# Kernel optimization log

Measured on AMD Instinct MI355X. Metric: run time of the kernel, lower is better.

Reference implementation:

```python
import jax, jax.numpy as jnp
import numpy as np

BETA = 0.99
EPS = 1e-05


def setup_inputs() -> dict:
    key = jax.random.key(0)
    s = jax.random.normal(key, (16, 2000, 257, 2), dtype=jnp.float32)
    return {"s": s}


def reference(s):
    # s: (N, T, F, C). Unbiased EWMA mean/var normalization, sequential over T.
    N, T, F, C = s.shape
    st = jnp.transpose(s, (1, 0, 2, 3))  # (T, N, F, C) for scan over time
    zeros = jnp.zeros((N, F, C), dtype=s.dtype)
    one = jnp.asarray(1.0, dtype=s.dtype)
    beta = jnp.asarray(BETA, dtype=s.dtype)

    def step(carry, x):
        beta_t, v1, v2, S = carry
        beta_t = beta * beta_t
        v1 = beta * v1 + (1 - beta) * x
        v2_prev = v2
        v2 = v1 / (1 - beta_t)
        w = (1 - beta) / (1 - beta_t)
        S = (1 - w) * S + w * (x - v2) * (x - v2_prev)
        S = S * (S > 0)  # clamp negative variance to 0 (as in original)
        y = (x - v2) / jnp.sqrt(S + EPS)
        return (beta_t, v1, v2, S), y

    init = (one, zeros, zeros, zeros)
    _, out = jax.lax.scan(step, init, st)
    return jnp.transpose(out, (1, 0, 2, 3))  # back to (N, T, F, C)
```

## Files before the change

### kernel.cpp

```cpp
#include <hip/hip_runtime.h>


#define NN 16
#define TT 2000
#define FCC 514
#define SERIES (NN * FCC)
#define EPSF 1e-5f
#define NCHUNK 7
#define CLEN 286
#define WARM 512
#define PF 16
#define MAXL 800

__global__ __launch_bounds__(64)
void ewma_kernel(const float* __restrict__ s, float* __restrict__ out) {
    __shared__ float4 tab[MAXL];

    const int chunk = blockIdx.y;
    const int t_out = chunk * CLEN;
    int t_end = t_out + CLEN; if (t_end > TT) t_end = TT;
    int t0 = t_out - WARM;     if (t0 < 0) t0 = 0;
    const int L = t_end - t0;

    {
        double bd = 0.99, acc = 1.0;
        int e = t0 + 1 + (int)threadIdx.x;
        while (e) { if (e & 1) acc *= bd; bd *= bd; e >>= 1; }
        double b64 = 0.99;
        for (int i = 0; i < 6; ++i) b64 *= b64;
        for (int j = (int)threadIdx.x; j < L; j += 64) {
            const float om = (float)(1.0 - acc);
            const float r  = __builtin_amdgcn_rcpf(om);
            const float w  = 0.01f * r;
            tab[j] = make_float4(r, w, 1.0f - w, 0.0f);
            acc *= b64;
        }
    }
    __syncthreads();

    const int tid = blockIdx.x * 64 + (int)threadIdx.x;
    if (tid >= SERIES) return;

    const int n  = tid / FCC;
    const int fc = tid - n * FCC;
    const size_t base = (size_t)n * TT * FCC + (size_t)fc + (size_t)t0 * FCC;
    const float* p  = s   + base;
    float*       po = out + base;

    float v1 = 0.0f, v2p = 0.0f, S = 0.0f;

    float buf[PF];
    #pragma unroll
    for (int i = 0; i < PF; ++i) buf[i] = p[i * FCC];

    int t = t0, j = 0;
    while (t + PF <= t_end) {
        const float* pf_ptr = (t + 2 * PF <= t_end) ? (p + PF * FCC) : p;
        float nbuf[PF];
        #pragma unroll
        for (int i = 0; i < PF; ++i) nbuf[i] = pf_ptr[i * FCC];

        const bool full_out = (t >= t_out);
        #pragma unroll
        for (int i = 0; i < PF; ++i) {
            const float4 tw = tab[j + i];
            const float x  = buf[i];
            v1 = fmaf(0.99f, v1, 0.01f * x);
            const float v2 = v1 * tw.x;
            const float d  = x - v2;
            const float pr = d * (x - v2p);
            S = fmaxf(fmaf(tw.z, S, tw.y * pr), 0.0f);
            const float y = d * __builtin_amdgcn_rsqf(S + EPSF);
            v2p = v2;
            if (full_out || (t + i >= t_out)) po[i * FCC] = y;
        }

        #pragma unroll
        for (int i = 0; i < PF; ++i) buf[i] = nbuf[i];
        p  += PF * FCC;
        po += PF * FCC;
        t  += PF;
        j  += PF;
    }
    for (; t < t_end; ++t, ++j) {
        const float4 tw = tab[j];
        const float x  = *p;
        v1 = fmaf(0.99f, v1, 0.01f * x);
        const float v2 = v1 * tw.x;
        const float d  = x - v2;
        const float pr = d * (x - v2p);
        S = fmaxf(fmaf(tw.z, S, tw.y * pr), 0.0f);
        const float y = d * __builtin_amdgcn_rsqf(S + EPSF);
        v2p = v2;
        if (t >= t_out) *po = y;
        p  += FCC;
        po += FCC;
    }
}

extern "C" void kernel_launch(void* const* d_in, const int* in_sizes, int n_in,
                              void* d_out, int out_size, void* d_ws, size_t ws_size,
                              hipStream_t stream) {
    const float* s = (const float*)d_in[0];
    float* out = (float*)d_out;
    dim3 grid((SERIES + 63) / 64, NCHUNK);
    ewma_kernel<<<grid, dim3(64), 0, stream>>>(s, out);
}
```

Measured before the change: 162.1 us.

## Stage time tiles through double-buffered LDS with cooperative float2 loads per batch

Each block now handles one batch element and one time chunk (16x16 grid, 576 threads). Threads cooperatively load contiguous tiles of 14 time steps x 514 features into double-buffered shared memory with float2 loads, while 514 threads run the recurrence out of LDS. Time chunks shrink to 125 steps with the same 512-step warmup, so redundant warmup work grows considerably in exchange for more parallelism and coalesced bulk loads. The weight table is reduced to float2 and the S update is rewritten as S + w*(pr - S).

```diff
diff --git a/kernel.cpp b/kernel.cpp
--- a/kernel.cpp
+++ b/kernel.cpp
@@ -1,100 +1,113 @@
 #include <hip/hip_runtime.h>
 
 
-#define NN 16
-#define TT 2000
-#define FCC 514
-#define SERIES (NN * FCC)
+#define NN   16
+#define TT   2000
+#define FCC  514
 #define EPSF 1e-5f
-#define NCHUNK 7
-#define CLEN 286
+#define KCH  16
+#define CLEN 125
 #define WARM 512
-#define PF 16
-#define MAXL 800
+#define TILE 14
+#define BLK  576
+#define MAXL (CLEN + WARM)
+#define ITER 7
 
-__global__ __launch_bounds__(64)
+__global__ __launch_bounds__(BLK)
 void ewma_kernel(const float* __restrict__ s, float* __restrict__ out) {
-    __shared__ float4 tab[MAXL];
+    __shared__ float  buf[2][TILE * FCC];
+    __shared__ float2 tab[MAXL];
 
-    const int chunk = blockIdx.y;
-    const int t_out = chunk * CLEN;
-    int t_end = t_out + CLEN; if (t_end > TT) t_end = TT;
-    int t0 = t_out - WARM;     if (t0 < 0) t0 = 0;
-    const int L = t_end - t0;
+    const int tid = (int)threadIdx.x;
+    const int c   = (int)blockIdx.x;
+    const int n   = (int)blockIdx.y;
+
+    const int t_out = c * CLEN;
+    const int t_end = t_out + CLEN;
+    int t0 = t_out - WARM; if (t0 < 0) t0 = 0;
+    const int L    = t_end - t0;
+    const int jout = t_out - t0;
+
+    for (int j = tid; j < L; j += BLK) {
+        double bd = 0.99, acc = 1.0;
+        int e = t0 + 1 + j;
+        while (e) { if (e & 1) acc *= bd; bd *= bd; e >>= 1; }
+        const float om = (float)(1.0 - acc);
+        const float r  = __builtin_amdgcn_rcpf(om);
+        tab[j] = make_float2(r, 0.01f * r);
+    }
+
+    const size_t base = (size_t)n * TT * FCC + (size_t)t0 * FCC;
+    const float* sb = s   + base;
+    float*       ob = out + base;
+
+    const int ntile = (L + TILE - 1) / TILE;
+
+    float2 pre[ITER];
 
     {
-        double bd = 0.99, acc = 1.0;
-        int e = t0 + 1 + (int)threadIdx.x;
-        while (e) { if (e & 1) acc *= bd; bd *= bd; e >>= 1; }
-        double b64 = 0.99;
-        for (int i = 0; i < 6; ++i) b64 *= b64;
-        for (int j = (int)threadIdx.x; j < L; j += 64) {
-            const float om = (float)(1.0 - acc);
-            const float r  = __builtin_amdgcn_rcpf(om);
-            const float w  = 0.01f * r;
-            tab[j] = make_float4(r, w, 1.0f - w, 0.0f);
-            acc *= b64;
+        const int navail = (L < TILE ? L : TILE) * FCC;
+        #pragma unroll
+        for (int it = 0; it < ITER; ++it) {
+            const int o = tid * 2 + it * (BLK * 2);
+            if (o < navail) pre[it] = *(const float2*)(sb + o);
+        }
+        #pragma unroll
+        for (int it = 0; it < ITER; ++it) {
+            const int o = tid * 2 + it * (BLK * 2);
+            if (o < navail) *(float2*)&buf[0][o] = pre[it];
         }
     }
     __syncthreads();
 
-    const int tid = blockIdx.x * 64 + (int)threadIdx.x;
-    if (tid >= SERIES) return;
+    float v1 = 0.f, v2p = 0.f, S = 0.f;
 
-    const int n  = tid / FCC;
-    const int fc = tid - n * FCC;
-    const size_t base = (size_t)n * TT * FCC + (size_t)fc + (size_t)t0 * FCC;
-    const float* p  = s   + base;
-    float*       po = out + base;
+    for (int k = 0; k < ntile; ++k) {
+        const int b    = k & 1;
+        const int rows = (L - k * TILE < TILE) ? (L - k * TILE) : TILE;
 
-    float v1 = 0.0f, v2p = 0.0f, S = 0.0f;
-
-    float buf[PF];
-    #pragma unroll
-    for (int i = 0; i < PF; ++i) buf[i] = p[i * FCC];
-
-    int t = t0, j = 0;
-    while (t + PF <= t_end) {
-        const float* pf_ptr = (t + 2 * PF <= t_end) ? (p + PF * FCC) : p;
-        float nbuf[PF];
-        #pragma unroll
-        for (int i = 0; i < PF; ++i) nbuf[i] = pf_ptr[i * FCC];
-
-        const bool full_out = (t >= t_out);
-        #pragma unroll
-        for (int i = 0; i < PF; ++i) {
-            const float4 tw = tab[j + i];
-            const float x  = buf[i];
-            v1 = fmaf(0.99f, v1, 0.01f * x);
-            const float v2 = v1 * tw.x;
-            const float d  = x - v2;
-            const float pr = d * (x - v2p);
-            S = fmaxf(fmaf(tw.z, S, tw.y * pr), 0.0f);
-            const float y = d * __builtin_amdgcn_rsqf(S + EPSF);
-            v2p = v2;
-            if (full_out || (t + i >= t_out)) po[i * FCC] = y;
+        int nnext = 0;
+        if (k + 1 < ntile) {
+            const int rn = (L - (k + 1) * TILE < TILE) ? (L - (k + 1) * TILE) : TILE;
+            nnext = rn * FCC;
+            const float* g = sb + (size_t)(k + 1) * TILE * FCC;
+            #pragma unroll
+            for (int it = 0; it < ITER; ++it) {
+                const int o = tid * 2 + it * (BLK * 2);
+                if (o < nnext) pre[it] = *(const float2*)(g + o);
+            }
         }
 
-        #pragma unroll
-        for (int i = 0; i < PF; ++i) buf[i] = nbuf[i];
-        p  += PF * FCC;
-        po += PF * FCC;
-        t  += PF;
-        j  += PF;
-    }
-    for (; t < t_end; ++t, ++j) {
-        const float4 tw = tab[j];
-        const float x  = *p;
-        v1 = fmaf(0.99f, v1, 0.01f * x);
-        const float v2 = v1 * tw.x;
-        const float d  = x - v2;
-        const float pr = d * (x - v2p);
-        S = fmaxf(fmaf(tw.z, S, tw.y * pr), 0.0f);
-        const float y = d * __builtin_amdgcn_rsqf(S + EPSF);
-        v2p = v2;
-        if (t >= t_out) *po = y;
-        p  += FCC;
-        po += FCC;
+        if (tid < FCC) {
+            const float* tp = &buf[b][tid];
+            float*       op = ob + (size_t)k * TILE * FCC + tid;
+            const int jb = k * TILE;
+            #pragma unroll
+            for (int r = 0; r < TILE; ++r) {
+                if (r < rows) {
+                    const float2 tw = tab[jb + r];
+                    const float x  = tp[r * FCC];
+                    v1 = fmaf(0.99f, v1, 0.01f * x);
+                    const float v2 = v1 * tw.x;
+                    const float d  = x - v2;
+                    const float pr = d * (x - v2p);
+                    S = fmaxf(fmaf(tw.y, pr - S, S), 0.f);
+                    const float y = d * __builtin_amdgcn_rsqf(S + EPSF);
+                    v2p = v2;
+                    if (jb + r >= jout) op[r * FCC] = y;
+                }
+            }
+        }
+
+        if (k + 1 < ntile) {
+            float* dst = &buf[1 - b][0];
+            #pragma unroll
+            for (int it = 0; it < ITER; ++it) {
+                const int o = tid * 2 + it * (BLK * 2);
+                if (o < nnext) *(float2*)&dst[o] = pre[it];
+            }
+        }
+        __syncthreads();
     }
 }
 
@@ -103,6 +116,6 @@
                               hipStream_t stream) {
     const float* s = (const float*)d_in[0];
     float* out = (float*)d_out;
-    dim3 grid((SERIES + 63) / 64, NCHUNK);
-    ewma_kernel<<<grid, dim3(64), 0, stream>>>(s, out);
+    dim3 grid(KCH, NN);
+    ewma_kernel<<<grid, dim3(BLK), 0, stream>>>(s, out);
 }
```

Result: slower. 254.7 us (+57.1%).
